# Kernel tuning notes

Hardware: AMD Instinct MI355X
Metric: run time of the kernel (lower is better)

## Reference

```python
import jax, jax.numpy as jnp
import numpy as np

D_MODEL = 1024
NHEAD = 16
HEAD_DIM = D_MODEL // NHEAD
D_FF = 4096
EPS = 1e-5


def _layer_norm(x, g, b):
    mu = jnp.mean(x, axis=-1, keepdims=True)
    var = jnp.mean((x - mu) ** 2, axis=-1, keepdims=True)
    return (x - mu) * jax.lax.rsqrt(var + EPS) * g + b


def _rotate_every_two(x):
    x1 = x[..., ::2]
    x2 = x[..., 1::2]
    return jnp.stack([-x2, x1], axis=-1).reshape(x.shape)


def _rope_cos_sin(pos_start, length, head_dim, dtype):
    inv_freq = 1.0 / (10000.0 ** (jnp.arange(0, head_dim, 2, dtype=jnp.float32) / head_dim))
    pos = jnp.arange(pos_start, pos_start + length, dtype=jnp.float32)
    ang = jnp.einsum('i,j->ij', pos, inv_freq)  # (len, head_dim/2)
    cos = jnp.repeat(jnp.cos(ang), 2, axis=-1).astype(dtype)
    sin = jnp.repeat(jnp.sin(ang), 2, axis=-1).astype(dtype)
    return cos, sin


def setup_inputs() -> dict:
    key = jax.random.key(0)
    ks = jax.random.split(key, 16)
    s = 1.0 / np.sqrt(D_MODEL)
    sf = 1.0 / np.sqrt(D_FF)
    inp = {
        'src': jax.random.normal(ks[0], (2048, 2, D_MODEL), jnp.float32),
        'src_mask': jnp.ones((2048, 2048), jnp.float32),
        'Wq': jax.random.normal(ks[1], (D_MODEL, D_MODEL), jnp.float32) * s,
        'bq': jnp.zeros((D_MODEL,), jnp.float32),
        'Wk': jax.random.normal(ks[2], (D_MODEL, D_MODEL), jnp.float32) * s,
        'bk': jnp.zeros((D_MODEL,), jnp.float32),
        'Wv': jax.random.normal(ks[3], (D_MODEL, D_MODEL), jnp.float32) * s,
        'bv': jnp.zeros((D_MODEL,), jnp.float32),
        'Wo': jax.random.normal(ks[4], (D_MODEL, D_MODEL), jnp.float32) * s,
        'bo': jnp.zeros((D_MODEL,), jnp.float32),
        'W1': jax.random.normal(ks[5], (D_MODEL, D_FF), jnp.float32) * s,
        'b1': jnp.zeros((D_FF,), jnp.float32),
        'W2': jax.random.normal(ks[6], (D_FF, D_MODEL), jnp.float32) * sf,
        'b2': jnp.zeros((D_MODEL,), jnp.float32),
        'g1': jnp.ones((D_MODEL,), jnp.float32),
        'be1': jnp.zeros((D_MODEL,), jnp.float32),
        'g2': jnp.ones((D_MODEL,), jnp.float32),
        'be2': jnp.zeros((D_MODEL,), jnp.float32),
    }
    return inp


def _attention(q, k, v, attn_mask):
    # q, k, v: (S, B, D) already projected
    s, b, _ = q.shape
    kl = k.shape[0]

    def heads(x):
        # (L, B, D) -> (B, H, L, dh)
        return x.reshape(x.shape[0], b, NHEAD, HEAD_DIM).transpose(1, 2, 0, 3)

    qh, kh, vh = heads(q), heads(k), heads(v)
    q_cos, q_sin = _rope_cos_sin(0, s, HEAD_DIM, qh.dtype)
    k_cos, k_sin = _rope_cos_sin(0, kl, HEAD_DIM, kh.dtype)
    qh = qh * q_cos + _rotate_every_two(qh) * q_sin
    kh = kh * k_cos + _rotate_every_two(kh) * k_sin

    scores = jnp.einsum('bhqd,bhkd->bhqk', qh, kh) / np.sqrt(HEAD_DIM)
    if attn_mask is not None:
        scores = jnp.where(attn_mask[None, None, :, :] < 0.1, -jnp.inf, scores)
    w = jax.nn.softmax(scores, axis=-1)
    out = jnp.einsum('bhqk,bhkd->bhqd', w, vh)  # (B, H, S, dh)
    out = out.transpose(2, 0, 1, 3).reshape(s, b, D_MODEL)
    return out


def reference(src, src_mask, Wq, bq, Wk, bk, Wv, bv, Wo, bo, W1, b1, W2, b2, g1, be1, g2, be2):
    q = src @ Wq + bq
    k = src @ Wk + bk
    v = src @ Wv + bv
    attn = _attention(q, k, v, src_mask) @ Wo + bo
    src2 = _layer_norm(src + attn, g1, be1)
    ff = jax.nn.relu(src2 @ W1 + b1) @ W2 + b2
    out = _layer_norm(src2 + ff, g2, be2)
    return out
```

## Files before the change

### kernel.cpp

```cpp
#include <hip/hip_runtime.h>
#include <math.h>

#define S_LEN 2048
#define DM 1024
#define NH 16
#define HD 64
#define DFF 4096
#define MROWS 4096

typedef unsigned short u16;
typedef __attribute__((ext_vector_type(8))) __bf16 bf16x8;
typedef __attribute__((ext_vector_type(4))) float f32x4;
typedef __attribute__((ext_vector_type(16))) float f32x16;
typedef __attribute__((ext_vector_type(4))) int int32x4;

__device__ __forceinline__ u16 f2bf(float f) {
  unsigned u = __float_as_uint(f);
  unsigned r = (u + 0x7fffu + ((u >> 16) & 1u)) >> 16;
  return (u16)r;
}

__device__ __forceinline__ float bf2f(u16 u) {
  return __uint_as_float((unsigned)u << 16);
}

__device__ __forceinline__ unsigned cvtpk_bf16(float lo, float hi) {
  unsigned r;
  asm("v_cvt_pk_bf16_f32 %0, %1, %2" : "=v"(r) : "v"(lo), "v"(hi));
  return r;
}

__device__ __forceinline__ void gload_lds16(const void* g, void* l) {
  __builtin_amdgcn_global_load_lds((__attribute__((address_space(1))) void*)g,
                                   (__attribute__((address_space(3))) void*)l, 16, 0, 0);
}

__global__ __launch_bounds__(256) void k_transpose_bf16(const float* __restrict__ W,
                                                        u16* __restrict__ Wt, int K, int N) {
  __shared__ float tile[32][33];
  int n0 = blockIdx.x * 32, k0 = blockIdx.y * 32;
  int tx = threadIdx.x & 31, ty = threadIdx.x >> 5;
  #pragma unroll
  for (int r = ty; r < 32; r += 8) tile[r][tx] = W[(size_t)(k0 + r) * N + n0 + tx];
  __syncthreads();
  #pragma unroll
  for (int r = ty; r < 32; r += 8) Wt[(size_t)(n0 + r) * K + k0 + tx] = f2bf(tile[tx][r]);
}

__global__ __launch_bounds__(256) void k_f2bf4(const float4* __restrict__ in,
                                               ushort4* __restrict__ out, int n4) {
  int i = blockIdx.x * 256 + threadIdx.x;
  if (i >= n4) return;
  float4 v = in[i];
  ushort4 o;
  o.x = f2bf(v.x); o.y = f2bf(v.y); o.z = f2bf(v.z); o.w = f2bf(v.w);
  out[i] = o;
}

__global__ __launch_bounds__(256) void k_rope_table(float* __restrict__ cosT,
                                                    float* __restrict__ sinT) {
  int idx = blockIdx.x * 256 + threadIdx.x;
  if (idx >= S_LEN * 32) return;
  int s = idx >> 5, i = idx & 31;
  float inv = powf(10000.f, -(float)(2 * i) / 64.f);
  float ang = (float)s * inv;
  cosT[idx] = cosf(ang);
  sinT[idx] = sinf(ang);
}

__global__ __launch_bounds__(256) void k_cat3(const float* __restrict__ a, const float* __restrict__ b,
                                              const float* __restrict__ c, float* __restrict__ o) {
  int i = blockIdx.x * 256 + threadIdx.x;
  if (i >= 3072) return;
  o[i] = i < 1024 ? a[i] : (i < 2048 ? b[i - 1024] : c[i - 2048]);
}

__global__ __launch_bounds__(256) void k_mask_flags(const float* __restrict__ mask,
                                                    unsigned char* __restrict__ flags) {
  int kt = blockIdx.x, qt = blockIdx.y;
  const float* mp = mask + (size_t)(qt * 64) * S_LEN + kt * 64;
  int tr = threadIdx.x >> 2;
  int tc = (threadIdx.x & 3) * 16;
  int ok = 1;
  #pragma unroll
  for (int c = 0; c < 16; c += 4) {
    float4 v = *(const float4*)(mp + (size_t)tr * S_LEN + tc + c);
    ok &= (v.x >= 0.1f) & (v.y >= 0.1f) & (v.z >= 0.1f) & (v.w >= 0.1f);
  }
  ok = __all(ok) ? 1 : 0;
  __shared__ int sh[4];
  if ((threadIdx.x & 63) == 0) sh[threadIdx.x >> 6] = ok;
  __syncthreads();
  if (threadIdx.x == 0) flags[qt * 32 + kt] = (sh[0] & sh[1] & sh[2] & sh[3]) ? 0 : 1;
}

enum { EPI_F32 = 0, EPI_RELU_BF16 = 2, EPI_PARTB = 4 };

template <int EPI>
__global__ __launch_bounds__(512, 2) void k_gemm256(const u16* __restrict__ A,
                                                    const u16* __restrict__ Bt,
                                                    const float* __restrict__ bias,
                                                    float* __restrict__ Cf, u16* __restrict__ Cb,
                                                    int M, int N, int K, int ldc, int Kc) {
  __shared__ __attribute__((aligned(16))) u16 As[4][256 * 32];
  __shared__ __attribute__((aligned(16))) u16 Bs[4][256 * 32];

  int nx = gridDim.x;
  int nwg = nx * gridDim.y;
  int flat = blockIdx.y * nx + blockIdx.x;
  int id = (flat & 7) * (nwg >> 3) + (flat >> 3);
  int n0 = (id % nx) * 256;
  int m0 = (id / nx) * 256;
  int kz = blockIdx.z * Kc;

  int tid = threadIdx.x;
  int lane = tid & 63, w = tid >> 6;
  int wm = (w >> 2) * 128, wn = (w & 3) * 64;
  int l15 = lane & 15, l4 = lane >> 4;
  int NT = Kc >> 5;

  const u16* aS[2];
  const u16* bS[2];
  int dslot[2];
  #pragma unroll
  for (int j = 0; j < 2; ++j) {
    int P = j * 512 + tid;
    int r = P >> 2;
    int sl = (P & 3) ^ (r & 3);
    aS[j] = A + (size_t)(m0 + r) * K + kz + sl * 8;
    bS[j] = Bt + (size_t)(n0 + r) * K + kz + sl * 8;
    dslot[j] = j * 512 + w * 64;
  }

  f32x4 acc[8][4] = {};

  #pragma unroll
  for (int t = 0; t < 3; ++t) {
    #pragma unroll
    for (int j = 0; j < 2; ++j) {
      gload_lds16(aS[j] + t * 32, &As[t][dslot[j] * 8]);
      gload_lds16(bS[j] + t * 32, &Bs[t][dslot[j] * 8]);
    }
  }

  for (int t = 0; t < NT; ++t) {
    int buf = t & 3;
    if (t < NT - 2) asm volatile("s_waitcnt vmcnt(8)" ::: "memory");
    else if (t == NT - 2) asm volatile("s_waitcnt vmcnt(4)" ::: "memory");
    else asm volatile("s_waitcnt vmcnt(0)" ::: "memory");
    __builtin_amdgcn_s_barrier();

    if (t + 3 < NT) {
      int tn = t + 3;
      int bn = tn & 3;
      #pragma unroll
      for (int j = 0; j < 2; ++j) {
        gload_lds16(aS[j] + tn * 32, &As[bn][dslot[j] * 8]);
        gload_lds16(bS[j] + tn * 32, &Bs[bn][dslot[j] * 8]);
      }
    }

    bf16x8 af[8], bq[4];
    #pragma unroll
    for (int m = 0; m < 8; ++m) {
      int r = wm + m * 16 + l15;
      af[m] = *(const bf16x8*)&As[buf][r * 32 + (l4 ^ (r & 3)) * 8];
    }
    #pragma unroll
    for (int n = 0; n < 4; ++n) {
      int r = wn + n * 16 + l15;
      bq[n] = *(const bf16x8*)&Bs[buf][r * 32 + (l4 ^ (r & 3)) * 8];
    }
    __builtin_amdgcn_s_setprio(1);
    #pragma unroll
    for (int m = 0; m < 8; ++m)
      #pragma unroll
      for (int n = 0; n < 4; ++n)
        acc[m][n] = __builtin_amdgcn_mfma_f32_16x16x32_bf16(af[m], bq[n], acc[m][n], 0, 0, 0);
    __builtin_amdgcn_s_setprio(0);
  }

  size_t zoff = (size_t)blockIdx.z * M * ldc;
  #pragma unroll
  for (int m = 0; m < 8; ++m) {
    #pragma unroll
    for (int n = 0; n < 4; ++n) {
      int col = n0 + wn + n * 16 + l15;
      float bv = (EPI == EPI_PARTB) ? 0.f : bias[col];
      #pragma unroll
      for (int r = 0; r < 4; ++r) {
        int row = m0 + wm + m * 16 + l4 * 4 + r;
        float v = acc[m][n][r] + bv;
        size_t o = (size_t)row * ldc + col;
        if (EPI == EPI_F32) Cf[o] = v;
        else if (EPI == EPI_RELU_BF16) Cb[o] = f2bf(fmaxf(v, 0.f));
        else Cb[zoff + o] = f2bf(v);
      }
    }
  }
}

#define QSCALE 0.180336881f
__global__ __launch_bounds__(256) void k_rope_heads(const float* __restrict__ QKV,
                                                    const float* __restrict__ cosT,
                                                    const float* __restrict__ sinT,
                                                    u16* __restrict__ Qh, u16* __restrict__ Kh,
                                                    u16* __restrict__ Vt) {
  int idx = blockIdx.x * 256 + threadIdx.x;
  if (idx >= MROWS * 512) return;
  int m = idx >> 9, c2 = idx & 511;
  int h = c2 >> 5, i = c2 & 31, d = 2 * i;
  int s = m >> 1, b = m & 1;
  int bh = b * NH + h;
  size_t base = (size_t)m * 3072 + h * 64 + d;
  float q0 = QKV[base], q1 = QKV[base + 1];
  float k0 = QKV[base + 1024], k1 = QKV[base + 1025];
  float v0 = QKV[base + 2048], v1 = QKV[base + 2049];
  float c = cosT[s * 32 + i], sn = sinT[s * 32 + i];
  size_t ho = ((size_t)bh * S_LEN + s) * 64 + d;
  Qh[ho]     = f2bf((q0 * c - q1 * sn) * QSCALE);
  Qh[ho + 1] = f2bf((q1 * c + q0 * sn) * QSCALE);
  Kh[ho]     = f2bf(k0 * c - k1 * sn);
  Kh[ho + 1] = f2bf(k1 * c + k0 * sn);
  size_t vo = ((size_t)bh * 64 + d) * S_LEN + s;
  Vt[vo] = f2bf(v0);
  Vt[vo + S_LEN] = f2bf(v1);
}

__global__ __launch_bounds__(256) void k_attn(const u16* __restrict__ Qh, const u16* __restrict__ Kh,
                                              const u16* __restrict__ Vt,
                                              const float* __restrict__ mask,
                                              const unsigned char* __restrict__ flags,
                                              u16* __restrict__ Out) {
  __shared__ __attribute__((aligned(16))) u16 Ks[128 * 64];
  __shared__ __attribute__((aligned(16))) u16 Vs[64 * 128];
  int bh = blockIdx.y;
  int q0 = blockIdx.x * 128;
  int b = bh >> 4, h = bh & 15;
  int tid = threadIdx.x, lane = tid & 63, w = tid >> 6;
  int l31 = lane & 31, l5 = lane >> 5;

  int qrow = q0 + w * 32 + l31;
  int qt = qrow >> 6;

  bf16x8 qf[4];
  {
    const u16* qp = Qh + ((size_t)bh * S_LEN + qrow) * 64 + l5 * 8;
    #pragma unroll
    for (int dc = 0; dc < 4; ++dc) qf[dc] = *(const bf16x8*)(qp + dc * 16);
  }

  float m_run = -1e30f, l_run = 0.f;
  f32x16 oA = {}, oB = {};

  for (int kv0 = 0; kv0 < S_LEN; kv0 += 128) {
    __syncthreads();
    #pragma unroll
    for (int i = 0; i < 4; ++i) {
      int sid = i * 256 + tid;
      int kr = sid >> 3, kslot = sid & 7;
      gload_lds16(Kh + ((size_t)bh * S_LEN + kv0 + kr) * 64 + (kslot ^ (kr & 7)) * 8, &Ks[sid * 8]);
      int vr = sid >> 4, vslot = sid & 15;
      gload_lds16(Vt + ((size_t)bh * 64 + vr) * S_LEN + kv0 + ((vslot ^ (vr & 15))) * 8, &Vs[sid * 8]);
    }
    __syncthreads();

    #pragma unroll
    for (int ksub = 0; ksub < 2; ++ksub) {
      int koff = ksub * 64;
      f32x16 sA = {}, sB = {};
      #pragma unroll
      for (int dc = 0; dc < 4; ++dc) {
        int r0 = koff + l31;
        int r1 = koff + 32 + l31;
        int slot = (dc * 2 + l5) ^ (l31 & 7);
        bf16x8 ka0 = *(const bf16x8*)&Ks[r0 * 64 + slot * 8];
        bf16x8 ka1 = *(const bf16x8*)&Ks[r1 * 64 + slot * 8];
        sA = __builtin_amdgcn_mfma_f32_32x32x16_bf16(ka0, qf[dc], sA, 0, 0, 0);
        sB = __builtin_amdgcn_mfma_f32_32x32x16_bf16(ka1, qf[dc], sB, 0, 0, 0);
      }

      int fl = flags[qt * 32 + ((kv0 + koff) >> 6)];
      if (fl) {
        const float* mrow = mask + (size_t)qrow * S_LEN + kv0 + koff;
        #pragma unroll
        for (int r = 0; r < 16; ++r) {
          int key = (r & 3) + 8 * (r >> 2) + 4 * l5;
          if (mrow[key] < 0.1f) sA[r] = -1e30f;
          if (mrow[key + 32] < 0.1f) sB[r] = -1e30f;
        }
      }

      float pm = m_run;
      #pragma unroll
      for (int r = 0; r < 16; ++r) pm = fmaxf(pm, fmaxf(sA[r], sB[r]));
      pm = fmaxf(pm, __shfl_xor(pm, 32, 64));
      if (!__all(pm <= m_run + 8.f)) {
        float corr = __builtin_amdgcn_exp2f(m_run - pm);
        m_run = pm;
        l_run *= corr;
        #pragma unroll
        for (int r = 0; r < 16; ++r) { oA[r] *= corr; oB[r] *= corr; }
      }
      float ps = 0.f;
      #pragma unroll
      for (int r = 0; r < 16; ++r) {
        sA[r] = __builtin_amdgcn_exp2f(sA[r] - m_run);
        sB[r] = __builtin_amdgcn_exp2f(sB[r] - m_run);
        ps += sA[r] + sB[r];
      }
      l_run += ps;

      #pragma unroll
      for (int kh = 0; kh < 2; ++kh) {
        f32x16 s = kh ? sB : sA;
        #pragma unroll
        for (int c = 0; c < 2; ++c) {
          int base = c * 8;
          unsigned u0 = cvtpk_bf16(s[base + 0], s[base + 1]);
          unsigned u1 = cvtpk_bf16(s[base + 2], s[base + 3]);
          unsigned u2 = cvtpk_bf16(s[base + 4], s[base + 5]);
          unsigned u3 = cvtpk_bf16(s[base + 6], s[base + 7]);
          asm volatile("v_permlane32_swap_b32 %0, %1" : "+v"(u0), "+v"(u2));
          asm volatile("v_permlane32_swap_b32 %0, %1" : "+v"(u1), "+v"(u3));
          int32x4 wds = {(int)u0, (int)u1, (int)u2, (int)u3};
          bf16x8 pb = *(bf16x8*)&wds;
          int kslot = ksub * 8 + (kh * 2 + c) * 2 + l5;
          int vr0 = l31, vr1 = 32 + l31;
          bf16x8 va0 = *(const bf16x8*)&Vs[vr0 * 128 + (kslot ^ (vr0 & 15)) * 8];
          bf16x8 va1 = *(const bf16x8*)&Vs[vr1 * 128 + (kslot ^ (vr1 & 15)) * 8];
          oA = __builtin_amdgcn_mfma_f32_32x32x16_bf16(va0, pb, oA, 0, 0, 0);
          oB = __builtin_amdgcn_mfma_f32_32x32x16_bf16(va1, pb, oB, 0, 0, 0);
        }
      }
    }
  }

  float l_tot = l_run + __shfl_xor(l_run, 32, 64);
  float inv = 1.f / l_tot;
  int mrow = qrow * 2 + b;
  u16* op = Out + (size_t)mrow * DM + h * 64;
  #pragma unroll
  for (int db = 0; db < 2; ++db) {
    f32x16 o = db ? oB : oA;
    #pragma unroll
    for (int g = 0; g < 4; ++g) {
      int d0 = db * 32 + 8 * g + 4 * l5;
      ushort4 st;
      st.x = f2bf(o[4 * g + 0] * inv);
      st.y = f2bf(o[4 * g + 1] * inv);
      st.z = f2bf(o[4 * g + 2] * inv);
      st.w = f2bf(o[4 * g + 3] * inv);
      *(ushort4*)(op + d0) = st;
    }
  }
}

__device__ __forceinline__ float wave_sum(float v) {
  #pragma unroll
  for (int off = 32; off >= 1; off >>= 1) v += __shfl_xor(v, off, 64);
  return v;
}

template <int WB>
__global__ __launch_bounds__(256) void k_lnp(const u16* __restrict__ pb, const float* __restrict__ addf,
                                             const float* __restrict__ bvec,
                                             const float* __restrict__ gw, const float* __restrict__ bw,
                                             float* __restrict__ Yf, u16* __restrict__ Yb) {
  int m = blockIdx.x;
  int tid = threadIdx.x, lane = tid & 63, w = tid >> 6;
  __shared__ float part[4];
  __shared__ float shv[2];
  float4 sc = ((const float4*)(addf + (size_t)m * DM))[tid];
  float4 bv = ((const float4*)bvec)[tid];
  float vx = sc.x + bv.x, vy = sc.y + bv.y, vz = sc.z + bv.z, vw = sc.w + bv.w;
  #pragma unroll
  for (int z = 0; z < 4; ++z) {
    ushort4 qv = ((const ushort4*)(pb + (size_t)z * MROWS * DM + (size_t)m * DM))[tid];
    vx += bf2f(qv.x); vy += bf2f(qv.y); vz += bf2f(qv.z); vw += bf2f(qv.w);
  }
  float s = wave_sum(vx + vy + vz + vw);
  if (lane == 0) part[w] = s;
  __syncthreads();
  if (tid == 0) shv[0] = (part[0] + part[1] + part[2] + part[3]) * (1.f / DM);
  __syncthreads();
  float mu = shv[0];
  float d0 = vx - mu, d1 = vy - mu, d2 = vz - mu, d3 = vw - mu;
  float q = wave_sum(d0 * d0 + d1 * d1 + d2 * d2 + d3 * d3);
  if (lane == 0) part[w] = q;
  __syncthreads();
  if (tid == 0) shv[1] = rsqrtf((part[0] + part[1] + part[2] + part[3]) * (1.f / DM) + 1e-5f);
  __syncthreads();
  float rstd = shv[1];
  float4 g4 = ((const float4*)gw)[tid];
  float4 b4 = ((const float4*)bw)[tid];
  float y0 = d0 * rstd * g4.x + b4.x;
  float y1 = d1 * rstd * g4.y + b4.y;
  float y2 = d2 * rstd * g4.z + b4.z;
  float y3 = d3 * rstd * g4.w + b4.w;
  ((float4*)(Yf + (size_t)m * DM))[tid] = make_float4(y0, y1, y2, y3);
  if (WB) {
    ushort4 o;
    o.x = f2bf(y0); o.y = f2bf(y1); o.z = f2bf(y2); o.w = f2bf(y3);
    ((ushort4*)(Yb + (size_t)m * DM))[tid] = o;
  }
}

extern "C" void kernel_launch(void* const* d_in, const int* in_sizes, int n_in,
                              void* d_out, int out_size, void* d_ws, size_t ws_size,
                              hipStream_t stream) {
  (void)in_sizes; (void)n_in; (void)out_size; (void)ws_size;
  const float* src  = (const float*)d_in[0];
  const float* mask = (const float*)d_in[1];
  const float* Wq = (const float*)d_in[2];  const float* bq  = (const float*)d_in[3];
  const float* Wk = (const float*)d_in[4];  const float* bk  = (const float*)d_in[5];
  const float* Wv = (const float*)d_in[6];  const float* bv  = (const float*)d_in[7];
  const float* Wo = (const float*)d_in[8];  const float* bo  = (const float*)d_in[9];
  const float* W1 = (const float*)d_in[10]; const float* b1  = (const float*)d_in[11];
  const float* W2 = (const float*)d_in[12]; const float* b2  = (const float*)d_in[13];
  const float* g1 = (const float*)d_in[14]; const float* be1 = (const float*)d_in[15];
  const float* g2 = (const float*)d_in[16]; const float* be2 = (const float*)d_in[17];
  float* out = (float*)d_out;

  char* base = (char*)d_ws;
  size_t off = 0;
  auto carve = [&](size_t bytes) -> void* {
    void* r = base + off;
    off += (bytes + 255) & ~(size_t)255;
    return r;
  };
  u16* Wq_t = (u16*)carve(2ull * 1024 * 1024);
  u16* Wk_t = (u16*)carve(2ull * 1024 * 1024);
  u16* Wv_t = (u16*)carve(2ull * 1024 * 1024);
  u16* Wo_t = (u16*)carve(2ull * 1024 * 1024);
  u16* W1_t = (u16*)carve(2ull * 4096 * 1024);
  u16* W2_t = (u16*)carve(2ull * 1024 * 4096);
  u16* Xbf  = (u16*)carve(2ull * 4096 * 1024);
  float* cosT = (float*)carve(4ull * 2048 * 32);
  float* sinT = (float*)carve(4ull * 2048 * 32);
  float* bqkv = (float*)carve(4ull * 3072);
  unsigned char* mflags = (unsigned char*)carve(1024);
  u16* attn_out = (u16*)carve(2ull * 4096 * 1024);
  float* src2f = (float*)carve(4ull * 4096 * 1024);
  float* QKV = (float*)carve(4ull * 4096 * 3072);
  u16* Qh = (u16*)carve(2ull * 32 * 2048 * 64);
  u16* Kh = (u16*)carve(2ull * 32 * 2048 * 64);
  u16* Vt = (u16*)carve(2ull * 32 * 2048 * 64);
  u16* woPb = (u16*)QKV;
  u16* ff1 = (u16*)QKV;
  u16* ffPb = (u16*)((char*)QKV + 32ull * 1024 * 1024);
  u16* src2b = (u16*)Vt;

  dim3 blk(256);
  dim3 blk5(512);
  k_transpose_bf16<<<dim3(32, 32), blk, 0, stream>>>(Wq, Wq_t, 1024, 1024);
  k_transpose_bf16<<<dim3(32, 32), blk, 0, stream>>>(Wk, Wk_t, 1024, 1024);
  k_transpose_bf16<<<dim3(32, 32), blk, 0, stream>>>(Wv, Wv_t, 1024, 1024);
  k_transpose_bf16<<<dim3(32, 32), blk, 0, stream>>>(Wo, Wo_t, 1024, 1024);
  k_transpose_bf16<<<dim3(128, 32), blk, 0, stream>>>(W1, W1_t, 1024, 4096);
  k_transpose_bf16<<<dim3(32, 128), blk, 0, stream>>>(W2, W2_t, 4096, 1024);
  k_f2bf4<<<dim3(4096), blk, 0, stream>>>((const float4*)src, (ushort4*)Xbf, 4096 * 1024 / 4);
  k_rope_table<<<dim3(256), blk, 0, stream>>>(cosT, sinT);
  k_cat3<<<dim3(12), blk, 0, stream>>>(bq, bk, bv, bqkv);
  k_mask_flags<<<dim3(32, 32), blk, 0, stream>>>(mask, mflags);
  k_gemm256<EPI_F32><<<dim3(12, 16, 1), blk5, 0, stream>>>(Xbf, Wq_t, bqkv, QKV, nullptr, 4096, 3072, 1024, 3072, 1024);
  k_rope_heads<<<dim3(MROWS * 512 / 256), blk, 0, stream>>>(QKV, cosT, sinT, Qh, Kh, Vt);
  k_attn<<<dim3(16, 32), blk, 0, stream>>>(Qh, Kh, Vt, mask, mflags, attn_out);
  k_gemm256<EPI_PARTB><<<dim3(4, 16, 4), blk5, 0, stream>>>(attn_out, Wo_t, nullptr, nullptr, woPb, 4096, 1024, 1024, 1024, 256);
  k_lnp<1><<<dim3(4096), blk, 0, stream>>>(woPb, src, bo, g1, be1, src2f, src2b);
  k_gemm256<EPI_RELU_BF16><<<dim3(16, 16, 1), blk5, 0, stream>>>(src2b, W1_t, b1, nullptr, ff1, 4096, 4096, 1024, 4096, 1024);
  k_gemm256<EPI_PARTB><<<dim3(4, 16, 4), blk5, 0, stream>>>(ff1, W2_t, nullptr, nullptr, ffPb, 4096, 1024, 4096, 1024, 1024);
  k_lnp<0><<<dim3(4096), blk, 0, stream>>>(ffPb, src2f, b2, g2, be2, out, nullptr);
}
```

Baseline: 316.4 us.

## Double-buffer attention K/V tiles, emit bf16 QKV, remap attn blocks, batch transposes

The attention kernel now double-buffers K and V tiles in shared memory, issuing the next tile's async global-to-LDS loads before computing on the current one, so memory latency overlaps with MFMA work. Attention blocks are remapped so each XCD handles a contiguous set of heads, which should improve L2 reuse of K/V. The QKV projection GEMM writes bf16 instead of fp32, halving that intermediate's traffic, and the rope kernel reads bf16. The four square weight transposes are merged into one launch. The costs are extra rounding of Q/K/V before rope and doubled attention LDS use, which may reduce occupancy.

```diff
diff --git a/kernel.cpp b/kernel.cpp
--- a/kernel.cpp
+++ b/kernel.cpp
@@ -33,6 +33,22 @@
 __device__ __forceinline__ void gload_lds16(const void* g, void* l) {
   __builtin_amdgcn_global_load_lds((__attribute__((address_space(1))) void*)g,
                                    (__attribute__((address_space(3))) void*)l, 16, 0, 0);
+}
+
+__global__ __launch_bounds__(256) void k_transpose4(const float* __restrict__ W0, const float* __restrict__ W1,
+                                                    const float* __restrict__ W2, const float* __restrict__ W3,
+                                                    u16* __restrict__ T0, u16* __restrict__ T1,
+                                                    u16* __restrict__ T2, u16* __restrict__ T3) {
+  __shared__ float tile[32][33];
+  const float* W = blockIdx.z == 0 ? W0 : blockIdx.z == 1 ? W1 : blockIdx.z == 2 ? W2 : W3;
+  u16* Wt = blockIdx.z == 0 ? T0 : blockIdx.z == 1 ? T1 : blockIdx.z == 2 ? T2 : T3;
+  int n0 = blockIdx.x * 32, k0 = blockIdx.y * 32;
+  int tx = threadIdx.x & 31, ty = threadIdx.x >> 5;
+  #pragma unroll
+  for (int r = ty; r < 32; r += 8) tile[r][tx] = W[(size_t)(k0 + r) * 1024 + n0 + tx];
+  __syncthreads();
+  #pragma unroll
+  for (int r = ty; r < 32; r += 8) Wt[(size_t)(n0 + r) * 1024 + k0 + tx] = f2bf(tile[tx][r]);
 }
 
 __global__ __launch_bounds__(256) void k_transpose_bf16(const float* __restrict__ W,
@@ -94,7 +110,7 @@
   if (threadIdx.x == 0) flags[qt * 32 + kt] = (sh[0] & sh[1] & sh[2] & sh[3]) ? 0 : 1;
 }
 
-enum { EPI_F32 = 0, EPI_RELU_BF16 = 2, EPI_PARTB = 4 };
+enum { EPI_F32 = 0, EPI_RELU_BF16 = 2, EPI_PARTB = 4, EPI_BF16 = 5 };
 
 template <int EPI>
 __global__ __launch_bounds__(512, 2) void k_gemm256(const u16* __restrict__ A,
@@ -194,6 +210,7 @@
         size_t o = (size_t)row * ldc + col;
         if (EPI == EPI_F32) Cf[o] = v;
         else if (EPI == EPI_RELU_BF16) Cb[o] = f2bf(fmaxf(v, 0.f));
+        else if (EPI == EPI_BF16) Cb[o] = f2bf(v);
         else Cb[zoff + o] = f2bf(v);
       }
     }
@@ -201,7 +218,7 @@
 }
 
 #define QSCALE 0.180336881f
-__global__ __launch_bounds__(256) void k_rope_heads(const float* __restrict__ QKV,
+__global__ __launch_bounds__(256) void k_rope_heads(const u16* __restrict__ QKVb,
                                                     const float* __restrict__ cosT,
                                                     const float* __restrict__ sinT,
                                                     u16* __restrict__ Qh, u16* __restrict__ Kh,
@@ -213,9 +230,9 @@
   int s = m >> 1, b = m & 1;
   int bh = b * NH + h;
   size_t base = (size_t)m * 3072 + h * 64 + d;
-  float q0 = QKV[base], q1 = QKV[base + 1];
-  float k0 = QKV[base + 1024], k1 = QKV[base + 1025];
-  float v0 = QKV[base + 2048], v1 = QKV[base + 2049];
+  float q0 = bf2f(QKVb[base]), q1 = bf2f(QKVb[base + 1]);
+  float k0 = bf2f(QKVb[base + 1024]), k1 = bf2f(QKVb[base + 1025]);
+  float v0 = bf2f(QKVb[base + 2048]), v1 = bf2f(QKVb[base + 2049]);
   float c = cosT[s * 32 + i], sn = sinT[s * 32 + i];
   size_t ho = ((size_t)bh * S_LEN + s) * 64 + d;
   Qh[ho]     = f2bf((q0 * c - q1 * sn) * QSCALE);
@@ -232,10 +249,12 @@
                                               const float* __restrict__ mask,
                                               const unsigned char* __restrict__ flags,
                                               u16* __restrict__ Out) {
-  __shared__ __attribute__((aligned(16))) u16 Ks[128 * 64];
-  __shared__ __attribute__((aligned(16))) u16 Vs[64 * 128];
-  int bh = blockIdx.y;
-  int q0 = blockIdx.x * 128;
+  __shared__ __attribute__((aligned(16))) u16 Ks[2][128 * 64];
+  __shared__ __attribute__((aligned(16))) u16 Vs[2][64 * 128];
+  int f = blockIdx.y * gridDim.x + blockIdx.x;
+  int xcd = f & 7, ii = f >> 3;
+  int bh = xcd * 4 + (ii >> 4);
+  int q0 = (ii & 15) * 128;
   int b = bh >> 4, h = bh & 15;
   int tid = threadIdx.x, lane = tid & 63, w = tid >> 6;
   int l31 = lane & 31, l5 = lane >> 5;
@@ -250,20 +269,46 @@
     for (int dc = 0; dc < 4; ++dc) qf[dc] = *(const bf16x8*)(qp + dc * 16);
   }
 
+  const u16* Kbase = Kh + (size_t)bh * S_LEN * 64;
+  const u16* Vbase = Vt + (size_t)bh * 64 * S_LEN;
+
+  int ksid[4], vsid[4];
+  const u16* kg[4];
+  const u16* vg[4];
+  #pragma unroll
+  for (int i = 0; i < 4; ++i) {
+    int sid = i * 256 + tid;
+    ksid[i] = sid;
+    int kr = sid >> 3, kslot = sid & 7;
+    kg[i] = Kbase + (size_t)kr * 64 + (kslot ^ (kr & 7)) * 8;
+    vsid[i] = sid;
+    int vr = sid >> 4, vslot = sid & 15;
+    vg[i] = Vbase + (size_t)vr * S_LEN + ((vslot ^ (vr & 15))) * 8;
+  }
+
   float m_run = -1e30f, l_run = 0.f;
   f32x16 oA = {}, oB = {};
 
-  for (int kv0 = 0; kv0 < S_LEN; kv0 += 128) {
-    __syncthreads();
-    #pragma unroll
-    for (int i = 0; i < 4; ++i) {
-      int sid = i * 256 + tid;
-      int kr = sid >> 3, kslot = sid & 7;
-      gload_lds16(Kh + ((size_t)bh * S_LEN + kv0 + kr) * 64 + (kslot ^ (kr & 7)) * 8, &Ks[sid * 8]);
-      int vr = sid >> 4, vslot = sid & 15;
-      gload_lds16(Vt + ((size_t)bh * 64 + vr) * S_LEN + kv0 + ((vslot ^ (vr & 15))) * 8, &Vs[sid * 8]);
-    }
-    __syncthreads();
+  const int NTILE = S_LEN / 128;
+  #pragma unroll
+  for (int i = 0; i < 4; ++i) {
+    gload_lds16(kg[i], &Ks[0][ksid[i] * 8]);
+    gload_lds16(vg[i], &Vs[0][vsid[i] * 8]);
+  }
+
+  for (int t = 0; t < NTILE; ++t) {
+    int cur = t & 1;
+    int kv0 = t * 128;
+    asm volatile("s_waitcnt vmcnt(0)" ::: "memory");
+    __builtin_amdgcn_s_barrier();
+    if (t + 1 < NTILE) {
+      int kvn = (t + 1) * 128;
+      #pragma unroll
+      for (int i = 0; i < 4; ++i) {
+        gload_lds16(kg[i] + (size_t)kvn * 64, &Ks[cur ^ 1][ksid[i] * 8]);
+        gload_lds16(vg[i] + kvn, &Vs[cur ^ 1][vsid[i] * 8]);
+      }
+    }
 
     #pragma unroll
     for (int ksub = 0; ksub < 2; ++ksub) {
@@ -274,8 +319,8 @@
         int r0 = koff + l31;
         int r1 = koff + 32 + l31;
         int slot = (dc * 2 + l5) ^ (l31 & 7);
-        bf16x8 ka0 = *(const bf16x8*)&Ks[r0 * 64 + slot * 8];
-        bf16x8 ka1 = *(const bf16x8*)&Ks[r1 * 64 + slot * 8];
+        bf16x8 ka0 = *(const bf16x8*)&Ks[cur][r0 * 64 + slot * 8];
+        bf16x8 ka1 = *(const bf16x8*)&Ks[cur][r1 * 64 + slot * 8];
         sA = __builtin_amdgcn_mfma_f32_32x32x16_bf16(ka0, qf[dc], sA, 0, 0, 0);
         sB = __builtin_amdgcn_mfma_f32_32x32x16_bf16(ka1, qf[dc], sB, 0, 0, 0);
       }
@@ -327,8 +372,8 @@
           bf16x8 pb = *(bf16x8*)&wds;
           int kslot = ksub * 8 + (kh * 2 + c) * 2 + l5;
           int vr0 = l31, vr1 = 32 + l31;
-          bf16x8 va0 = *(const bf16x8*)&Vs[vr0 * 128 + (kslot ^ (vr0 & 15)) * 8];
-          bf16x8 va1 = *(const bf16x8*)&Vs[vr1 * 128 + (kslot ^ (vr1 & 15)) * 8];
+          bf16x8 va0 = *(const bf16x8*)&Vs[cur][vr0 * 128 + (kslot ^ (vr0 & 15)) * 8];
+          bf16x8 va1 = *(const bf16x8*)&Vs[cur][vr1 * 128 + (kslot ^ (vr1 & 15)) * 8];
           oA = __builtin_amdgcn_mfma_f32_32x32x16_bf16(va0, pb, oA, 0, 0, 0);
           oB = __builtin_amdgcn_mfma_f32_32x32x16_bf16(va1, pb, oB, 0, 0, 0);
         }
@@ -446,6 +491,7 @@
   u16* Qh = (u16*)carve(2ull * 32 * 2048 * 64);
   u16* Kh = (u16*)carve(2ull * 32 * 2048 * 64);
   u16* Vt = (u16*)carve(2ull * 32 * 2048 * 64);
+  u16* QKVb = (u16*)QKV;
   u16* woPb = (u16*)QKV;
   u16* ff1 = (u16*)QKV;
   u16* ffPb = (u16*)((char*)QKV + 32ull * 1024 * 1024);
@@ -453,18 +499,15 @@
 
   dim3 blk(256);
   dim3 blk5(512);
-  k_transpose_bf16<<<dim3(32, 32), blk, 0, stream>>>(Wq, Wq_t, 1024, 1024);
-  k_transpose_bf16<<<dim3(32, 32), blk, 0, stream>>>(Wk, Wk_t, 1024, 1024);
-  k_transpose_bf16<<<dim3(32, 32), blk, 0, stream>>>(Wv, Wv_t, 1024, 1024);
-  k_transpose_bf16<<<dim3(32, 32), blk, 0, stream>>>(Wo, Wo_t, 1024, 1024);
+  k_transpose4<<<dim3(32, 32, 4), blk, 0, stream>>>(Wq, Wk, Wv, Wo, Wq_t, Wk_t, Wv_t, Wo_t);
   k_transpose_bf16<<<dim3(128, 32), blk, 0, stream>>>(W1, W1_t, 1024, 4096);
   k_transpose_bf16<<<dim3(32, 128), blk, 0, stream>>>(W2, W2_t, 4096, 1024);
   k_f2bf4<<<dim3(4096), blk, 0, stream>>>((const float4*)src, (ushort4*)Xbf, 4096 * 1024 / 4);
   k_rope_table<<<dim3(256), blk, 0, stream>>>(cosT, sinT);
   k_cat3<<<dim3(12), blk, 0, stream>>>(bq, bk, bv, bqkv);
   k_mask_flags<<<dim3(32, 32), blk, 0, stream>>>(mask, mflags);
-  k_gemm256<EPI_F32><<<dim3(12, 16, 1), blk5, 0, stream>>>(Xbf, Wq_t, bqkv, QKV, nullptr, 4096, 3072, 1024, 3072, 1024);
-  k_rope_heads<<<dim3(MROWS * 512 / 256), blk, 0, stream>>>(QKV, cosT, sinT, Qh, Kh, Vt);
+  k_gemm256<EPI_BF16><<<dim3(12, 16, 1), blk5, 0, stream>>>(Xbf, Wq_t, bqkv, nullptr, QKVb, 4096, 3072, 1024, 3072, 1024);
+  k_rope_heads<<<dim3(MROWS * 512 / 256), blk, 0, stream>>>(QKVb, cosT, sinT, Qh, Kh, Vt);
   k_attn<<<dim3(16, 32), blk, 0, stream>>>(Qh, Kh, Vt, mask, mflags, attn_out);
   k_gemm256<EPI_PARTB><<<dim3(4, 16, 4), blk5, 0, stream>>>(attn_out, Wo_t, nullptr, nullptr, woPb, 4096, 1024, 1024, 1024, 256);
   k_lnp<1><<<dim3(4096), blk, 0, stream>>>(woPb, src, bo, g1, be1, src2f, src2b);
```

Result: faster. 302.3 us (-4.4%).
